# Performance work log

Hardware: AMD Instinct MI355X
Metric: run time of the kernel (lower is better)

The kernel has to match this reference:

```python
import jax, jax.numpy as jnp
import numpy as np

B, T, D, E, I = 4, 2048, 2048, 8, 1024
TOP_K = 2
AUX_COEFF = 0.01


def setup_inputs() -> dict:
    key = jax.random.key(0)
    kx, kg, k1, k3, k2 = jax.random.split(key, 5)
    scale = 0.02
    x = jax.random.normal(kx, (B, T, D), dtype=jnp.float32)
    gate_w = jax.random.normal(kg, (E, D), dtype=jnp.float32) * scale   # nn.Linear weight [out,in]
    w1 = jax.random.normal(k1, (E, I, D), dtype=jnp.float32) * scale    # gate_proj per expert
    w3 = jax.random.normal(k3, (E, I, D), dtype=jnp.float32) * scale    # up_proj per expert
    w2 = jax.random.normal(k2, (E, D, I), dtype=jnp.float32) * scale    # down_proj per expert
    return {"x": x, "gate_w": gate_w, "w1": w1, "w3": w3, "w2": w2}


def reference(x, gate_w, w1, w3, w2):
    b, t, d = x.shape
    e = gate_w.shape[0]
    xf = x.reshape(b * t, d)                                   # [N, D]
    logits = xf @ gate_w.T                                     # [N, E]
    scores = jax.nn.softmax(logits, axis=-1)
    top_scores, top_idx = jax.lax.top_k(scores, TOP_K)         # [N, K]
    top_scores = top_scores / jnp.sum(top_scores, axis=-1, keepdims=True)
    # load-balancing aux loss (Switch Transformer)
    expert_mask = jax.nn.one_hot(top_idx, e, dtype=x.dtype).sum(axis=1)  # [N, E]
    f = expert_mask.mean(axis=0)
    p = scores.mean(axis=0)
    aux_loss = AUX_COEFF * e * jnp.sum(f * p)
    # dense all-expert SwiGLU (matches torch module's dense dispatch)
    h = jax.nn.silu(jnp.einsum('td,eid->tei', xf, w1)) * jnp.einsum('td,eid->tei', xf, w3)  # [N,E,I]
    expert_outs = jnp.einsum('tei,edi->ted', h, w2)            # [N, E, D]
    selected = jnp.take_along_axis(expert_outs, top_idx[:, :, None], axis=1)  # [N, K, D]
    out = jnp.sum(selected * top_scores[:, :, None], axis=1)   # [N, D]
    return out.reshape(b, t, d), aux_loss
```

## Files before the change

kernel.cpp:

```cpp
#include <hip/hip_runtime.h>
#include <hip/hip_bf16.h>

constexpr int kN = 8192;
constexpr int kD = 2048;
constexpr int kE = 8;
constexpr int kI = 1024;

typedef __bf16 bf16x8 __attribute__((ext_vector_type(8)));
typedef float  f32x4  __attribute__((ext_vector_type(4)));

constexpr size_t OFF_COUNTS = 0;
constexpr size_t OFF_PSUM   = 64;
constexpr size_t OFF_OFFS   = 128;
constexpr size_t OFF_CURSOR = 192;
constexpr size_t OFF_TOPE   = 256;
constexpr size_t OFF_TOPW   = OFF_TOPE + (size_t)kN * 8;
constexpr size_t OFF_SLOT   = OFF_TOPW + (size_t)kN * 8;
constexpr size_t OFF_TOK    = OFF_SLOT + (size_t)kN * 8;
constexpr size_t OFF_XB     = OFF_TOK + (size_t)kN * 8;
constexpr size_t OFF_W1B    = OFF_XB  + (size_t)kN * kD * 2;
constexpr size_t OFF_W3B    = OFF_W1B + (size_t)kE * kI * kD * 2;
constexpr size_t OFF_W2B    = OFF_W3B + (size_t)kE * kI * kD * 2;
constexpr size_t OFF_H      = OFF_W2B + (size_t)kE * kD * kI * 2;
constexpr size_t OFF_O2     = OFF_W1B;

typedef __attribute__((address_space(1))) const unsigned GU;
typedef __attribute__((address_space(3))) unsigned LU;
__device__ __forceinline__ void gload16(const void* g, void* l) {
    __builtin_amdgcn_global_load_lds((GU*)g, (LU*)l, 16, 0, 0);
}

__global__ __launch_bounds__(256) void convert_kernel(
    const float* __restrict__ src, __bf16* __restrict__ dst, int n8)
{
    int i = blockIdx.x * 256 + threadIdx.x;
    const int stride = gridDim.x * 256;
    for (; i < n8; i += stride) {
        const float4* s = (const float4*)(src + (size_t)i * 8);
        float4 f0 = s[0], f1 = s[1];
        bf16x8 v;
        v[0]=(__bf16)f0.x; v[1]=(__bf16)f0.y; v[2]=(__bf16)f0.z; v[3]=(__bf16)f0.w;
        v[4]=(__bf16)f1.x; v[5]=(__bf16)f1.y; v[6]=(__bf16)f1.z; v[7]=(__bf16)f1.w;
        *(bf16x8*)(dst + (size_t)i * 8) = v;
    }
}

__global__ __launch_bounds__(256) void gate_kernel(
    const float* __restrict__ x, const float* __restrict__ gw,
    unsigned* __restrict__ counts, float* __restrict__ psum,
    int2* __restrict__ tope, float2* __restrict__ topw,
    __bf16* __restrict__ xb)
{
    const int tid  = threadIdx.x;
    const int lane = tid & 63;
    const int wv   = tid >> 6;
    const int t    = blockIdx.x * 4 + wv;

    const float* xr = x + (size_t)t * kD;
    float xv[32];
#pragma unroll
    for (int j = 0; j < 32; ++j) xv[j] = xr[lane + 64 * j];

    __bf16* xbr = xb + (size_t)t * kD;
#pragma unroll
    for (int j = 0; j < 32; ++j) xbr[lane + 64 * j] = (__bf16)xv[j];

    float s[8];
#pragma unroll
    for (int e = 0; e < 8; ++e) {
        const float* gr = gw + (size_t)e * kD;
        float a = 0.f;
#pragma unroll
        for (int j = 0; j < 32; ++j) a += xv[j] * gr[lane + 64 * j];
        s[e] = a;
    }
#pragma unroll
    for (int off = 32; off > 0; off >>= 1) {
#pragma unroll
        for (int e = 0; e < 8; ++e) s[e] += __shfl_xor(s[e], off, 64);
    }
    float mx = s[0];
#pragma unroll
    for (int e = 1; e < 8; ++e) mx = fmaxf(mx, s[e]);
    float p[8]; float sum = 0.f;
#pragma unroll
    for (int e = 0; e < 8; ++e) { p[e] = expf(s[e] - mx); sum += p[e]; }
    float inv = 1.f / sum;
#pragma unroll
    for (int e = 0; e < 8; ++e) p[e] *= inv;

    int e0 = 0; float p0 = p[0];
#pragma unroll
    for (int e = 1; e < 8; ++e) if (p[e] > p0) { p0 = p[e]; e0 = e; }
    int e1 = -1; float p1 = -1.f;
#pragma unroll
    for (int e = 0; e < 8; ++e) if (e != e0 && p[e] > p1) { p1 = p[e]; e1 = e; }
    float wn = 1.f / (p0 + p1);

    __shared__ float ps[4][8];
    __shared__ unsigned cnt[8];
    if (tid < 8) cnt[tid] = 0u;
    __syncthreads();
    if (lane == 0) {
#pragma unroll
        for (int e = 0; e < 8; ++e) ps[wv][e] = p[e];
        atomicAdd(&cnt[e0], 1u);
        atomicAdd(&cnt[e1], 1u);
        tope[t] = make_int2(e0, e1);
        topw[t] = make_float2(p0 * wn, p1 * wn);
    }
    __syncthreads();
    if (tid < 8) {
        atomicAdd(&psum[tid], ps[0][tid] + ps[1][tid] + ps[2][tid] + ps[3][tid]);
        if (cnt[tid]) atomicAdd(&counts[tid], cnt[tid]);
    }
}

__global__ void scan_kernel(const unsigned* __restrict__ counts,
                            const float* __restrict__ psum,
                            unsigned* __restrict__ offs,
                            unsigned* __restrict__ cursor,
                            float* __restrict__ out)
{
    if (threadIdx.x == 0) {
        unsigned off = 0;
        float a = 0.f;
        for (int e = 0; e < 8; ++e) {
            offs[e] = off; cursor[e] = off; off += counts[e];
            a += ((float)counts[e] / (float)kN) * (psum[e] / (float)kN);
        }
        out[(size_t)kN * kD] = 0.01f * (float)kE * a;
    }
}

__global__ __launch_bounds__(256) void scatter_kernel(
    const int2* __restrict__ tope,
    unsigned* __restrict__ cursor, int* __restrict__ tok,
    int2* __restrict__ slotmap)
{
    int t = blockIdx.x * 256 + threadIdx.x;
    int2 ee = tope[t];
    unsigned q0 = atomicAdd(&cursor[ee.x], 1u);
    tok[q0] = t;
    unsigned q1 = atomicAdd(&cursor[ee.y], 1u);
    tok[q1] = t;
    slotmap[t] = make_int2((int)q0, (int)q1);
}

__global__ __launch_bounds__(256) void ffn_h_kernel(
    const __bf16* __restrict__ xb,
    const __bf16* __restrict__ w1b, const __bf16* __restrict__ w3b,
    const unsigned* __restrict__ counts, const unsigned* __restrict__ offs,
    const int* __restrict__ tok, __bf16* __restrict__ H)
{
    const int e  = blockIdx.z;
    const int mt = blockIdx.y;
    const int ct = blockIdx.x;
    const unsigned n_e = counts[e];
    if ((unsigned)(mt * 128) >= n_e) return;
    const unsigned base = offs[e];

    __shared__ __bf16 As[128][64];
    __shared__ __bf16 Bs[128][64];
    __shared__ int rowtok[128];

    const int tid  = threadIdx.x;
    const int lane = tid & 63;
    const int wv   = tid >> 6;
    const int wr   = wv >> 1, wc = wv & 1;

    if (tid < 128) {
        unsigned r = (unsigned)(mt * 128 + tid);
        rowtok[tid] = tok[base + (r < n_e ? r : 0u)];
    }
    __syncthreads();

    const __bf16* aptr[4];
    const __bf16* bptr[4];
    __bf16* alds[4];
    __bf16* blds[4];
#pragma unroll
    for (int j = 0; j < 4; ++j) {
        const int r = wv * 32 + j * 8 + (lane >> 3);
        const int c = (((lane & 7) ^ (r & 7)) << 3);
        aptr[j] = xb + (size_t)rowtok[r] * kD + c;
        alds[j] = &As[wv * 32 + j * 8][0];
        const int rr = r & 63;
        const int h  = ct * 64 + ((r >> 6) << 5) + (rr & 31);
        const __bf16* wsrc = (rr < 32) ? w1b : w3b;
        bptr[j] = wsrc + ((size_t)e * kI + h) * kD + c;
        blds[j] = &Bs[wv * 32 + j * 8][0];
    }

    f32x4 acc[4][4] = {};

    for (int k0 = 0; k0 < kD; k0 += 64) {
#pragma unroll
        for (int j = 0; j < 4; ++j) {
            gload16(aptr[j], alds[j]);
            gload16(bptr[j], blds[j]);
            aptr[j] += 64; bptr[j] += 64;
        }
        __syncthreads();

#pragma unroll
        for (int kk = 0; kk < 2; ++kk) {
            bf16x8 af[4];
#pragma unroll
            for (int m = 0; m < 4; ++m) {
                const int r = wr * 64 + m * 16 + (lane & 15);
                const int slot = (kk * 4 + (lane >> 4)) ^ (r & 7);
                af[m] = *(const bf16x8*)&As[r][slot << 3];
            }
#pragma unroll
            for (int n = 0; n < 4; ++n) {
                const int r = wc * 64 + n * 16 + (lane & 15);
                const int slot = (kk * 4 + (lane >> 4)) ^ (r & 7);
                bf16x8 bf = *(const bf16x8*)&Bs[r][slot << 3];
#pragma unroll
                for (int m = 0; m < 4; ++m)
                    acc[m][n] = __builtin_amdgcn_mfma_f32_16x16x32_bf16(af[m], bf, acc[m][n], 0, 0, 0);
            }
        }
        __syncthreads();
    }

    const int c0 = lane & 15;
    const int r0 = (lane >> 4) * 4;
    const int hbase = ct * 64 + wc * 32;
#pragma unroll
    for (int m = 0; m < 4; ++m) {
        const unsigned growb = (unsigned)(mt * 128 + wr * 64 + m * 16 + r0);
#pragma unroll
        for (int jj = 0; jj < 4; ++jj) {
            const unsigned grow = growb + jj;
            if (grow < n_e) {
                const size_t rowoff = (size_t)(base + grow) * kI;
#pragma unroll
                for (int n = 0; n < 2; ++n) {
                    float a1 = acc[m][n][jj];
                    float a3 = acc[m][n + 2][jj];
                    float h = a1 / (1.f + __expf(-a1)) * a3;
                    H[rowoff + hbase + n * 16 + c0] = (__bf16)h;
                }
            }
        }
    }
}

__global__ __launch_bounds__(256) void ffn_out_kernel(
    const __bf16* __restrict__ H, const __bf16* __restrict__ w2b,
    const unsigned* __restrict__ counts, const unsigned* __restrict__ offs,
    __bf16* __restrict__ O2)
{
    const int e  = blockIdx.z;
    const int mt = blockIdx.y;
    const int ct = blockIdx.x;
    const unsigned n_e = counts[e];
    if ((unsigned)(mt * 128) >= n_e) return;
    const unsigned base = offs[e];

    __shared__ __bf16 As[128][64];
    __shared__ __bf16 Bs[128][64];

    const int tid  = threadIdx.x;
    const int lane = tid & 63;
    const int wv   = tid >> 6;
    const int wr   = wv >> 1, wc = wv & 1;

    const __bf16* aptr[4];
    const __bf16* bptr[4];
    __bf16* alds[4];
    __bf16* blds[4];
#pragma unroll
    for (int j = 0; j < 4; ++j) {
        const int r = wv * 32 + j * 8 + (lane >> 3);
        const int c = (((lane & 7) ^ (r & 7)) << 3);
        const unsigned grow = (unsigned)(mt * 128 + r);
        const unsigned slot = base + (grow < n_e ? grow : 0u);
        aptr[j] = H + (size_t)slot * kI + c;
        alds[j] = &As[wv * 32 + j * 8][0];
        bptr[j] = w2b + ((size_t)e * kD + ct * 128 + r) * kI + c;
        blds[j] = &Bs[wv * 32 + j * 8][0];
    }

    f32x4 acc[4][4] = {};

    for (int k0 = 0; k0 < kI; k0 += 64) {
#pragma unroll
        for (int j = 0; j < 4; ++j) {
            gload16(aptr[j], alds[j]);
            gload16(bptr[j], blds[j]);
            aptr[j] += 64; bptr[j] += 64;
        }
        __syncthreads();

#pragma unroll
        for (int kk = 0; kk < 2; ++kk) {
            bf16x8 af[4];
#pragma unroll
            for (int m = 0; m < 4; ++m) {
                const int r = wr * 64 + m * 16 + (lane & 15);
                const int slot = (kk * 4 + (lane >> 4)) ^ (r & 7);
                af[m] = *(const bf16x8*)&As[r][slot << 3];
            }
#pragma unroll
            for (int n = 0; n < 4; ++n) {
                const int r = wc * 64 + n * 16 + (lane & 15);
                const int slot = (kk * 4 + (lane >> 4)) ^ (r & 7);
                bf16x8 bf = *(const bf16x8*)&Bs[r][slot << 3];
#pragma unroll
                for (int m = 0; m < 4; ++m)
                    acc[m][n] = __builtin_amdgcn_mfma_f32_16x16x32_bf16(af[m], bf, acc[m][n], 0, 0, 0);
            }
        }
        __syncthreads();
    }

    const int c0 = lane & 15;
    const int r0 = (lane >> 4) * 4;
#pragma unroll
    for (int m = 0; m < 4; ++m) {
#pragma unroll
        for (int jj = 0; jj < 4; ++jj) {
            const unsigned grow = (unsigned)(mt * 128 + wr * 64 + m * 16 + r0 + jj);
            if (grow < n_e) {
                __bf16* orow = O2 + (size_t)(base + grow) * kD + ct * 128 + wc * 64;
#pragma unroll
                for (int n = 0; n < 4; ++n)
                    orow[n * 16 + c0] = (__bf16)acc[m][n][jj];
            }
        }
    }
}

__global__ __launch_bounds__(256) void combine_kernel(
    const __bf16* __restrict__ O2, const int2* __restrict__ slotmap,
    const float2* __restrict__ topw, float* __restrict__ out)
{
    const int total = kN * (kD / 8);
    int i = blockIdx.x * 256 + threadIdx.x;
    const int stride = gridDim.x * 256;
    for (; i < total; i += stride) {
        const int t  = i >> 8;
        const int d8 = (i & 255) * 8;
        const int2   sm = slotmap[t];
        const float2 w  = topw[t];
        bf16x8 a = *(const bf16x8*)(O2 + (size_t)sm.x * kD + d8);
        bf16x8 b = *(const bf16x8*)(O2 + (size_t)sm.y * kD + d8);
        float r[8];
#pragma unroll
        for (int j = 0; j < 8; ++j)
            r[j] = w.x * (float)a[j] + w.y * (float)b[j];
        float4* o = (float4*)(out + (size_t)i * 8);
        o[0] = make_float4(r[0], r[1], r[2], r[3]);
        o[1] = make_float4(r[4], r[5], r[6], r[7]);
    }
}

extern "C" void kernel_launch(void* const* d_in, const int* in_sizes, int n_in,
                              void* d_out, int out_size, void* d_ws, size_t ws_size,
                              hipStream_t stream)
{
    const float* x  = (const float*)d_in[0];
    const float* gw = (const float*)d_in[1];
    const float* w1 = (const float*)d_in[2];
    const float* w3 = (const float*)d_in[3];
    const float* w2 = (const float*)d_in[4];
    float* out = (float*)d_out;
    char*  ws  = (char*)d_ws;

    unsigned* counts = (unsigned*)(ws + OFF_COUNTS);
    float*    psum   = (float*)(ws + OFF_PSUM);
    unsigned* offs   = (unsigned*)(ws + OFF_OFFS);
    unsigned* cursor = (unsigned*)(ws + OFF_CURSOR);
    int2*     tope   = (int2*)(ws + OFF_TOPE);
    float2*   topw   = (float2*)(ws + OFF_TOPW);
    int2*     slotmap= (int2*)(ws + OFF_SLOT);
    int*      tok    = (int*)(ws + OFF_TOK);
    __bf16*   xb     = (__bf16*)(ws + OFF_XB);
    __bf16*   w1b    = (__bf16*)(ws + OFF_W1B);
    __bf16*   w3b    = (__bf16*)(ws + OFF_W3B);
    __bf16*   w2b    = (__bf16*)(ws + OFF_W2B);
    __bf16*   H      = (__bf16*)(ws + OFF_H);
    __bf16*   O2     = (__bf16*)(ws + OFF_O2);

    hipMemsetAsync(d_ws, 0, 256, stream);

    gate_kernel<<<kN / 4, 256, 0, stream>>>(x, gw, counts, psum, tope, topw, xb);
    scan_kernel<<<1, 64, 0, stream>>>(counts, psum, offs, cursor, out);
    scatter_kernel<<<kN / 256, 256, 0, stream>>>(tope, cursor, tok, slotmap);

    const int n8w = kE * kI * kD / 8;
    convert_kernel<<<2048, 256, 0, stream>>>(w1, w1b, n8w);
    convert_kernel<<<2048, 256, 0, stream>>>(w3, w3b, n8w);
    convert_kernel<<<2048, 256, 0, stream>>>(w2, w2b, n8w);

    ffn_h_kernel<<<dim3(kI / 64, 2 * kN / 128, kE), 256, 0, stream>>>(
        xb, w1b, w3b, counts, offs, tok, H);
    ffn_out_kernel<<<dim3(kD / 128, 2 * kN / 128, kE), 256, 0, stream>>>(
        H, w2b, counts, offs, O2);
    combine_kernel<<<2048, 256, 0, stream>>>(O2, slotmap, topw, out);
}
```

Before: 569.7 us.

## Double-buffer LDS tiles in expert GEMMs and merge weight conversion launches

Both expert GEMM kernels now keep two LDS buffers for the A and B tiles. The next k-tile's global-to-LDS loads are issued before the MFMAs on the current tile, and one barrier per iteration is dropped. This is meant to hide global load latency behind compute, at the cost of doubling LDS per block (64KB), which may lower occupancy. The three weight fp32-to-bf16 conversion launches are also merged into one launch to cut launch overhead.

New measurement: 638.8 us. 1.12x slower.

```diff
diff --git a/kernel.cpp b/kernel.cpp
--- a/kernel.cpp
+++ b/kernel.cpp
@@ -30,12 +30,19 @@
     __builtin_amdgcn_global_load_lds((GU*)g, (LU*)l, 16, 0, 0);
 }
 
-__global__ __launch_bounds__(256) void convert_kernel(
-    const float* __restrict__ src, __bf16* __restrict__ dst, int n8)
-{
-    int i = blockIdx.x * 256 + threadIdx.x;
-    const int stride = gridDim.x * 256;
-    for (; i < n8; i += stride) {
+__global__ __launch_bounds__(256) void convert3_kernel(
+    const float* __restrict__ s0, const float* __restrict__ s1,
+    const float* __restrict__ s2,
+    __bf16* __restrict__ d0, __bf16* __restrict__ d1, __bf16* __restrict__ d2,
+    int n8seg)
+{
+    const int seg = blockIdx.x >> 11;
+    const int bid = blockIdx.x & 2047;
+    const float* src = (seg == 0) ? s0 : (seg == 1) ? s1 : s2;
+    __bf16*      dst = (seg == 0) ? d0 : (seg == 1) ? d1 : d2;
+    int i = bid * 256 + threadIdx.x;
+    const int stride = 2048 * 256;
+    for (; i < n8seg; i += stride) {
         const float4* s = (const float4*)(src + (size_t)i * 8);
         float4 f0 = s[0], f1 = s[1];
         bf16x8 v;
@@ -153,6 +160,7 @@
     const unsigned* __restrict__ counts, const unsigned* __restrict__ offs,
     const int* __restrict__ tok, __bf16* __restrict__ H)
 {
+    constexpr int NT = kD / 64;
     const int e  = blockIdx.z;
     const int mt = blockIdx.y;
     const int ct = blockIdx.x;
@@ -160,8 +168,8 @@
     if ((unsigned)(mt * 128) >= n_e) return;
     const unsigned base = offs[e];
 
-    __shared__ __bf16 As[128][64];
-    __shared__ __bf16 Bs[128][64];
+    __shared__ __bf16 As[2][128][64];
+    __shared__ __bf16 Bs[2][128][64];
     __shared__ int rowtok[128];
 
     const int tid  = threadIdx.x;
@@ -177,32 +185,37 @@
 
     const __bf16* aptr[4];
     const __bf16* bptr[4];
-    __bf16* alds[4];
-    __bf16* blds[4];
 #pragma unroll
     for (int j = 0; j < 4; ++j) {
         const int r = wv * 32 + j * 8 + (lane >> 3);
         const int c = (((lane & 7) ^ (r & 7)) << 3);
         aptr[j] = xb + (size_t)rowtok[r] * kD + c;
-        alds[j] = &As[wv * 32 + j * 8][0];
         const int rr = r & 63;
         const int h  = ct * 64 + ((r >> 6) << 5) + (rr & 31);
         const __bf16* wsrc = (rr < 32) ? w1b : w3b;
         bptr[j] = wsrc + ((size_t)e * kI + h) * kD + c;
-        blds[j] = &Bs[wv * 32 + j * 8][0];
     }
 
     f32x4 acc[4][4] = {};
 
-    for (int k0 = 0; k0 < kD; k0 += 64) {
-#pragma unroll
-        for (int j = 0; j < 4; ++j) {
-            gload16(aptr[j], alds[j]);
-            gload16(bptr[j], blds[j]);
-            aptr[j] += 64; bptr[j] += 64;
-        }
-        __syncthreads();
-
+#pragma unroll
+    for (int j = 0; j < 4; ++j) {
+        gload16(aptr[j], &As[0][wv * 32 + j * 8][0]);
+        gload16(bptr[j], &Bs[0][wv * 32 + j * 8][0]);
+        aptr[j] += 64; bptr[j] += 64;
+    }
+    __syncthreads();
+
+    int cur = 0;
+    for (int t = 0; t < NT; ++t) {
+        if (t + 1 < NT) {
+#pragma unroll
+            for (int j = 0; j < 4; ++j) {
+                gload16(aptr[j], &As[cur ^ 1][wv * 32 + j * 8][0]);
+                gload16(bptr[j], &Bs[cur ^ 1][wv * 32 + j * 8][0]);
+                aptr[j] += 64; bptr[j] += 64;
+            }
+        }
 #pragma unroll
         for (int kk = 0; kk < 2; ++kk) {
             bf16x8 af[4];
@@ -210,19 +223,20 @@
             for (int m = 0; m < 4; ++m) {
                 const int r = wr * 64 + m * 16 + (lane & 15);
                 const int slot = (kk * 4 + (lane >> 4)) ^ (r & 7);
-                af[m] = *(const bf16x8*)&As[r][slot << 3];
+                af[m] = *(const bf16x8*)&As[cur][r][slot << 3];
             }
 #pragma unroll
             for (int n = 0; n < 4; ++n) {
                 const int r = wc * 64 + n * 16 + (lane & 15);
                 const int slot = (kk * 4 + (lane >> 4)) ^ (r & 7);
-                bf16x8 bf = *(const bf16x8*)&Bs[r][slot << 3];
+                bf16x8 bf = *(const bf16x8*)&Bs[cur][r][slot << 3];
 #pragma unroll
                 for (int m = 0; m < 4; ++m)
                     acc[m][n] = __builtin_amdgcn_mfma_f32_16x16x32_bf16(af[m], bf, acc[m][n], 0, 0, 0);
             }
         }
-        __syncthreads();
+        if (t + 1 < NT) __syncthreads();
+        cur ^= 1;
     }
 
     const int c0 = lane & 15;
@@ -253,6 +267,7 @@
     const unsigned* __restrict__ counts, const unsigned* __restrict__ offs,
     __bf16* __restrict__ O2)
 {
+    constexpr int NT = kI / 64;
     const int e  = blockIdx.z;
     const int mt = blockIdx.y;
     const int ct = blockIdx.x;
@@ -260,8 +275,8 @@
     if ((unsigned)(mt * 128) >= n_e) return;
     const unsigned base = offs[e];
 
-    __shared__ __bf16 As[128][64];
-    __shared__ __bf16 Bs[128][64];
+    __shared__ __bf16 As[2][128][64];
+    __shared__ __bf16 Bs[2][128][64];
 
     const int tid  = threadIdx.x;
     const int lane = tid & 63;
@@ -270,8 +285,6 @@
 
     const __bf16* aptr[4];
     const __bf16* bptr[4];
-    __bf16* alds[4];
-    __bf16* blds[4];
 #pragma unroll
     for (int j = 0; j < 4; ++j) {
         const int r = wv * 32 + j * 8 + (lane >> 3);
@@ -279,22 +292,29 @@
         const unsigned grow = (unsigned)(mt * 128 + r);
         const unsigned slot = base + (grow < n_e ? grow : 0u);
         aptr[j] = H + (size_t)slot * kI + c;
-        alds[j] = &As[wv * 32 + j * 8][0];
         bptr[j] = w2b + ((size_t)e * kD + ct * 128 + r) * kI + c;
-        blds[j] = &Bs[wv * 32 + j * 8][0];
     }
 
     f32x4 acc[4][4] = {};
 
-    for (int k0 = 0; k0 < kI; k0 += 64) {
-#pragma unroll
-        for (int j = 0; j < 4; ++j) {
-            gload16(aptr[j], alds[j]);
-            gload16(bptr[j], blds[j]);
-            aptr[j] += 64; bptr[j] += 64;
-        }
-        __syncthreads();
-
+#pragma unroll
+    for (int j = 0; j < 4; ++j) {
+        gload16(aptr[j], &As[0][wv * 32 + j * 8][0]);
+        gload16(bptr[j], &Bs[0][wv * 32 + j * 8][0]);
+        aptr[j] += 64; bptr[j] += 64;
+    }
+    __syncthreads();
+
+    int cur = 0;
+    for (int t = 0; t < NT; ++t) {
+        if (t + 1 < NT) {
+#pragma unroll
+            for (int j = 0; j < 4; ++j) {
+                gload16(aptr[j], &As[cur ^ 1][wv * 32 + j * 8][0]);
+                gload16(bptr[j], &Bs[cur ^ 1][wv * 32 + j * 8][0]);
+                aptr[j] += 64; bptr[j] += 64;
+            }
+        }
 #pragma unroll
         for (int kk = 0; kk < 2; ++kk) {
             bf16x8 af[4];
@@ -302,19 +322,20 @@
             for (int m = 0; m < 4; ++m) {
                 const int r = wr * 64 + m * 16 + (lane & 15);
                 const int slot = (kk * 4 + (lane >> 4)) ^ (r & 7);
-                af[m] = *(const bf16x8*)&As[r][slot << 3];
+                af[m] = *(const bf16x8*)&As[cur][r][slot << 3];
             }
 #pragma unroll
             for (int n = 0; n < 4; ++n) {
                 const int r = wc * 64 + n * 16 + (lane & 15);
                 const int slot = (kk * 4 + (lane >> 4)) ^ (r & 7);
-                bf16x8 bf = *(const bf16x8*)&Bs[r][slot << 3];
+                bf16x8 bf = *(const bf16x8*)&Bs[cur][r][slot << 3];
 #pragma unroll
                 for (int m = 0; m < 4; ++m)
                     acc[m][n] = __builtin_amdgcn_mfma_f32_16x16x32_bf16(af[m], bf, acc[m][n], 0, 0, 0);
             }
         }
-        __syncthreads();
+        if (t + 1 < NT) __syncthreads();
+        cur ^= 1;
     }
 
     const int c0 = lane & 15;
@@ -391,10 +412,8 @@
     scan_kernel<<<1, 64, 0, stream>>>(counts, psum, offs, cursor, out);
     scatter_kernel<<<kN / 256, 256, 0, stream>>>(tope, cursor, tok, slotmap);
 
-    const int n8w = kE * kI * kD / 8;
-    convert_kernel<<<2048, 256, 0, stream>>>(w1, w1b, n8w);
-    convert_kernel<<<2048, 256, 0, stream>>>(w3, w3b, n8w);
-    convert_kernel<<<2048, 256, 0, stream>>>(w2, w2b, n8w);
+    convert3_kernel<<<3 * 2048, 256, 0, stream>>>(
+        w1, w3, w2, w1b, w3b, w2b, kE * kI * kD / 8);
 
     ffn_h_kernel<<<dim3(kI / 64, 2 * kN / 128, kE), 256, 0, stream>>>(
         xb, w1b, w3b, counts, offs, tok, H);
```

## Pre-gather routed tokens into contiguous bf16 buffer and merge weight conversions

Applied to the files above, without the earlier changes.

Removes the bf16 copy of x written in the gate kernel and adds a gather kernel that converts x rows directly into a per-expert contiguous bf16 buffer ordered by slot. The first FFN GEMM then reads A rows contiguously instead of doing indirect row lookups through a token table, which also drops a shared-memory preload and a barrier. The three weight-conversion launches are merged into one kernel. In exchange, an extra pass writes a buffer twice the size of x, and padding rows now clamp to the last valid row.

Measured after the change: 551.0 us. 1.03x faster.

```diff
diff --git a/kernel.cpp b/kernel.cpp
--- a/kernel.cpp
+++ b/kernel.cpp
@@ -17,12 +17,12 @@
 constexpr size_t OFF_TOPW   = OFF_TOPE + (size_t)kN * 8;
 constexpr size_t OFF_SLOT   = OFF_TOPW + (size_t)kN * 8;
 constexpr size_t OFF_TOK    = OFF_SLOT + (size_t)kN * 8;
-constexpr size_t OFF_XB     = OFF_TOK + (size_t)kN * 8;
-constexpr size_t OFF_W1B    = OFF_XB  + (size_t)kN * kD * 2;
+constexpr size_t OFF_XG     = OFF_TOK + (size_t)kN * 8;
+constexpr size_t OFF_W1B    = OFF_XG  + (size_t)2 * kN * kD * 2;
 constexpr size_t OFF_W3B    = OFF_W1B + (size_t)kE * kI * kD * 2;
 constexpr size_t OFF_W2B    = OFF_W3B + (size_t)kE * kI * kD * 2;
 constexpr size_t OFF_H      = OFF_W2B + (size_t)kE * kD * kI * 2;
-constexpr size_t OFF_O2     = OFF_W1B;
+constexpr size_t OFF_O2     = OFF_XG;
 
 typedef __attribute__((address_space(1))) const unsigned GU;
 typedef __attribute__((address_space(3))) unsigned LU;
@@ -30,12 +30,19 @@
     __builtin_amdgcn_global_load_lds((GU*)g, (LU*)l, 16, 0, 0);
 }
 
-__global__ __launch_bounds__(256) void convert_kernel(
-    const float* __restrict__ src, __bf16* __restrict__ dst, int n8)
-{
-    int i = blockIdx.x * 256 + threadIdx.x;
-    const int stride = gridDim.x * 256;
-    for (; i < n8; i += stride) {
+__global__ __launch_bounds__(256) void convert3_kernel(
+    const float* __restrict__ s0, const float* __restrict__ s1,
+    const float* __restrict__ s2,
+    __bf16* __restrict__ d0, __bf16* __restrict__ d1, __bf16* __restrict__ d2,
+    int n8seg)
+{
+    const int seg = blockIdx.x >> 11;
+    const int bid = blockIdx.x & 2047;
+    const float* src = (seg == 0) ? s0 : (seg == 1) ? s1 : s2;
+    __bf16*      dst = (seg == 0) ? d0 : (seg == 1) ? d1 : d2;
+    int i = bid * 256 + threadIdx.x;
+    const int stride = 2048 * 256;
+    for (; i < n8seg; i += stride) {
         const float4* s = (const float4*)(src + (size_t)i * 8);
         float4 f0 = s[0], f1 = s[1];
         bf16x8 v;
@@ -48,8 +55,7 @@
 __global__ __launch_bounds__(256) void gate_kernel(
     const float* __restrict__ x, const float* __restrict__ gw,
     unsigned* __restrict__ counts, float* __restrict__ psum,
-    int2* __restrict__ tope, float2* __restrict__ topw,
-    __bf16* __restrict__ xb)
+    int2* __restrict__ tope, float2* __restrict__ topw)
 {
     const int tid  = threadIdx.x;
     const int lane = tid & 63;
@@ -60,10 +66,6 @@
     float xv[32];
 #pragma unroll
     for (int j = 0; j < 32; ++j) xv[j] = xr[lane + 64 * j];
-
-    __bf16* xbr = xb + (size_t)t * kD;
-#pragma unroll
-    for (int j = 0; j < 32; ++j) xbr[lane + 64 * j] = (__bf16)xv[j];
 
     float s[8];
 #pragma unroll
@@ -147,11 +149,30 @@
     slotmap[t] = make_int2((int)q0, (int)q1);
 }
 
+__global__ __launch_bounds__(256) void gather_kernel(
+    const float* __restrict__ x, const int* __restrict__ tok,
+    __bf16* __restrict__ Xg)
+{
+    const int total = 2 * kN * (kD / 8);
+    int i = blockIdx.x * 256 + threadIdx.x;
+    const int stride = gridDim.x * 256;
+    for (; i < total; i += stride) {
+        const int slot = i >> 8;
+        const int d8   = (i & 255) * 8;
+        const float4* s = (const float4*)(x + (size_t)tok[slot] * kD + d8);
+        float4 f0 = s[0], f1 = s[1];
+        bf16x8 v;
+        v[0]=(__bf16)f0.x; v[1]=(__bf16)f0.y; v[2]=(__bf16)f0.z; v[3]=(__bf16)f0.w;
+        v[4]=(__bf16)f1.x; v[5]=(__bf16)f1.y; v[6]=(__bf16)f1.z; v[7]=(__bf16)f1.w;
+        *(bf16x8*)(Xg + (size_t)slot * kD + d8) = v;
+    }
+}
+
 __global__ __launch_bounds__(256) void ffn_h_kernel(
-    const __bf16* __restrict__ xb,
+    const __bf16* __restrict__ Xg,
     const __bf16* __restrict__ w1b, const __bf16* __restrict__ w3b,
     const unsigned* __restrict__ counts, const unsigned* __restrict__ offs,
-    const int* __restrict__ tok, __bf16* __restrict__ H)
+    __bf16* __restrict__ H)
 {
     const int e  = blockIdx.z;
     const int mt = blockIdx.y;
@@ -162,19 +183,12 @@
 
     __shared__ __bf16 As[128][64];
     __shared__ __bf16 Bs[128][64];
-    __shared__ int rowtok[128];
 
     const int tid  = threadIdx.x;
     const int lane = tid & 63;
     const int wv   = tid >> 6;
     const int wr   = wv >> 1, wc = wv & 1;
 
-    if (tid < 128) {
-        unsigned r = (unsigned)(mt * 128 + tid);
-        rowtok[tid] = tok[base + (r < n_e ? r : 0u)];
-    }
-    __syncthreads();
-
     const __bf16* aptr[4];
     const __bf16* bptr[4];
     __bf16* alds[4];
@@ -183,7 +197,9 @@
     for (int j = 0; j < 4; ++j) {
         const int r = wv * 32 + j * 8 + (lane >> 3);
         const int c = (((lane & 7) ^ (r & 7)) << 3);
-        aptr[j] = xb + (size_t)rowtok[r] * kD + c;
+        unsigned grow = (unsigned)(mt * 128 + r);
+        grow = grow < n_e ? grow : (n_e - 1);
+        aptr[j] = Xg + (size_t)(base + grow) * kD + c;
         alds[j] = &As[wv * 32 + j * 8][0];
         const int rr = r & 63;
         const int h  = ct * 64 + ((r >> 6) << 5) + (rr & 31);
@@ -276,9 +292,9 @@
     for (int j = 0; j < 4; ++j) {
         const int r = wv * 32 + j * 8 + (lane >> 3);
         const int c = (((lane & 7) ^ (r & 7)) << 3);
-        const unsigned grow = (unsigned)(mt * 128 + r);
-        const unsigned slot = base + (grow < n_e ? grow : 0u);
-        aptr[j] = H + (size_t)slot * kI + c;
+        unsigned grow = (unsigned)(mt * 128 + r);
+        grow = grow < n_e ? grow : (n_e - 1);
+        aptr[j] = H + (size_t)(base + grow) * kI + c;
         alds[j] = &As[wv * 32 + j * 8][0];
         bptr[j] = w2b + ((size_t)e * kD + ct * 128 + r) * kI + c;
         blds[j] = &Bs[wv * 32 + j * 8][0];
@@ -378,7 +394,7 @@
     float2*   topw   = (float2*)(ws + OFF_TOPW);
     int2*     slotmap= (int2*)(ws + OFF_SLOT);
     int*      tok    = (int*)(ws + OFF_TOK);
-    __bf16*   xb     = (__bf16*)(ws + OFF_XB);
+    __bf16*   Xg     = (__bf16*)(ws + OFF_XG);
     __bf16*   w1b    = (__bf16*)(ws + OFF_W1B);
     __bf16*   w3b    = (__bf16*)(ws + OFF_W3B);
     __bf16*   w2b    = (__bf16*)(ws + OFF_W2B);
@@ -387,17 +403,16 @@
 
     hipMemsetAsync(d_ws, 0, 256, stream);
 
-    gate_kernel<<<kN / 4, 256, 0, stream>>>(x, gw, counts, psum, tope, topw, xb);
+    gate_kernel<<<kN / 4, 256, 0, stream>>>(x, gw, counts, psum, tope, topw);
     scan_kernel<<<1, 64, 0, stream>>>(counts, psum, offs, cursor, out);
     scatter_kernel<<<kN / 256, 256, 0, stream>>>(tope, cursor, tok, slotmap);
 
-    const int n8w = kE * kI * kD / 8;
-    convert_kernel<<<2048, 256, 0, stream>>>(w1, w1b, n8w);
-    convert_kernel<<<2048, 256, 0, stream>>>(w3, w3b, n8w);
-    convert_kernel<<<2048, 256, 0, stream>>>(w2, w2b, n8w);
+    convert3_kernel<<<3 * 2048, 256, 0, stream>>>(
+        w1, w3, w2, w1b, w3b, w2b, kE * kI * kD / 8);
+    gather_kernel<<<2048, 256, 0, stream>>>(x, tok, Xg);
 
     ffn_h_kernel<<<dim3(kI / 64, 2 * kN / 128, kE), 256, 0, stream>>>(
-        xb, w1b, w3b, counts, offs, tok, H);
+        Xg, w1b, w3b, counts, offs, H);
     ffn_out_kernel<<<dim3(kD / 128, 2 * kN / 128, kE), 256, 0, stream>>>(
         H, w2b, counts, offs, O2);
     combine_kernel<<<2048, 256, 0, stream>>>(O2, slotmap, topw, out);
```
